# Performance work log

Hardware: AMD Instinct MI355X
Metric: run time of the kernel (lower is better)

## Reference

```python
import jax, jax.numpy as jnp
import numpy as np
import math

DIM = 1024
HEADS = 16
B, N = 2, 2048

POLY = jnp.array([-0.037, 0.481, -2.3, 4.917, -1.791], dtype=jnp.float32)


def adaptive_temperature_softmax(logits):
    # logits: [b, h, n, n]
    original_probs = jax.nn.softmax(logits, axis=-1)
    entropy = jnp.sum(-original_probs * jnp.log(original_probs + 1e-9), axis=-1, keepdims=True)
    e2 = entropy * entropy
    poly_result = POLY[0] * e2 * e2 + POLY[1] * e2 * entropy + POLY[2] * e2 + POLY[3] * entropy + POLY[4]
    beta = jnp.where(entropy > 0.5, jnp.maximum(poly_result, 1.0), 1.0)
    return jax.nn.softmax(logits * beta, axis=-1)


def setup_inputs() -> dict:
    key = jax.random.key(0)
    ks = jax.random.split(key, 5)
    s = 1.0 / math.sqrt(DIM)
    return {
        "x": jax.random.normal(ks[0], (B, N, DIM), dtype=jnp.float32),
        "Wq": jax.random.normal(ks[1], (DIM, DIM), dtype=jnp.float32) * s,
        "Wk": jax.random.normal(ks[2], (DIM, DIM), dtype=jnp.float32) * s,
        "Wv": jax.random.normal(ks[3], (DIM, DIM), dtype=jnp.float32) * s,
        "Wo": jax.random.normal(ks[4], (DIM, DIM), dtype=jnp.float32) * s,
        "bo": jnp.zeros((DIM,), dtype=jnp.float32),
    }


def reference(x, Wq, Wk, Wv, Wo, bo):
    b, n, d = x.shape
    h = HEADS
    hd = d // h
    # torch nn.Linear: y = x @ W.T (+ bias)
    def proj(W):
        t = x @ W.T  # [b, n, d]
        return t.reshape(b, n, h, hd).transpose(0, 2, 1, 3)  # [b, h, n, hd]
    q, k, v = proj(Wq), proj(Wk), proj(Wv)
    sim = jnp.einsum('bhid,bhjd->bhij', q, k) / math.sqrt(hd)
    neg = -jnp.finfo(sim.dtype).max
    causal = jnp.triu(jnp.ones((n, n), dtype=bool), k=1)  # True above diagonal
    sim = jnp.where(causal, neg, sim)
    attn = adaptive_temperature_softmax(sim)
    out = jnp.einsum('bhij,bhjd->bhid', attn, v)
    out = out.transpose(0, 2, 1, 3).reshape(b, n, d)
    return out @ Wo.T + bo
```

## Files before the change

### kernel.cpp

```cpp
#include <hip/hip_runtime.h>
#include <math.h>

#define B_   2
#define N_   2048
#define D_   1024
#define H_   16
#define HD_  64
#define BH_  32
#define M_   4096

typedef __bf16 bf16x8 __attribute__((ext_vector_type(8)));
typedef float  f32x4  __attribute__((ext_vector_type(4)));
typedef __attribute__((address_space(3))) uint  lds_u32;
typedef __attribute__((address_space(1))) uint  glob_u32;

__device__ inline unsigned short f2b(float f) {
    unsigned u = __float_as_uint(f);
    u += 0x7FFFu + ((u >> 16) & 1u);
    return (unsigned short)(u >> 16);
}
__device__ inline unsigned short f2b_fast(float f) {
    return (unsigned short)((__float_as_uint(f) + 0x8000u) >> 16);
}

__global__ __launch_bounds__(256)
void cvt_all(const float* __restrict__ x,  const float* __restrict__ wq,
             const float* __restrict__ wk, const float* __restrict__ wv,
             const float* __restrict__ wo, ushort* __restrict__ dst)
{
    int i = blockIdx.x * 256 + threadIdx.x;
    if (i >= 2097152) return;
    int fi = i * 4;
    const float* s; int off;
    if (fi < 4194304) { s = x; off = fi; }
    else {
        int r = fi - 4194304;
        int wsel = r >> 20;
        off = r & 1048575;
        s = (wsel == 0) ? wq : (wsel == 1) ? wk : (wsel == 2) ? wv : wo;
    }
    float4 f = *(const float4*)(s + off);
    ushort4 o;
    o.x = f2b(f.x); o.y = f2b(f.y); o.z = f2b(f.z); o.w = f2b(f.w);
    *(ushort4*)(dst + fi) = o;
}

template <int MODE>
__global__ __launch_bounds__(256)
void gemm_mfma(const ushort* __restrict__ A,
               const ushort* __restrict__ W0, const ushort* __restrict__ W1,
               const ushort* __restrict__ W2, const float* __restrict__ bias,
               ushort* __restrict__ O0, ushort* __restrict__ O1,
               ushort* __restrict__ O2, float* __restrict__ Of)
{
    const int z = blockIdx.z;
    const ushort* W = (z == 0) ? W0 : (z == 1) ? W1 : W2;

    __shared__ alignas(16) ushort As[128][32];
    __shared__ alignas(16) ushort Bs[128][32];

    const int t = threadIdx.x;
    const int lane = t & 63, w = t >> 6;
    const int quad = lane >> 4, l15 = lane & 15;
    const int wm = (w >> 1) * 64, wn = (w & 1) * 64;
    const int tileM = blockIdx.x * 128, tileN = blockIdx.y * 128;
    const int crow = lane >> 2;
    const int ccol = (lane & 3) * 8;

    f32x4 acc[4][4];
#pragma unroll
    for (int mt = 0; mt < 4; ++mt)
#pragma unroll
        for (int nt = 0; nt < 4; ++nt) acc[mt][nt] = (f32x4){0.f, 0.f, 0.f, 0.f};

    for (int k0 = 0; k0 < D_; k0 += 32) {
        __syncthreads();
#pragma unroll
        for (int cc = 0; cc < 2; ++cc) {
            int ch = w * 2 + cc;
            const ushort* ga = &A[(size_t)(tileM + ch * 16 + crow) * D_ + k0 + ccol];
            __builtin_amdgcn_global_load_lds((const glob_u32*)ga, (lds_u32*)&As[ch * 16][0], 16, 0, 0);
            const ushort* gb = &W[(size_t)(tileN + ch * 16 + crow) * D_ + k0 + ccol];
            __builtin_amdgcn_global_load_lds((const glob_u32*)gb, (lds_u32*)&Bs[ch * 16][0], 16, 0, 0);
        }
        __syncthreads();

        bf16x8 af[4], bf[4];
#pragma unroll
        for (int mt = 0; mt < 4; ++mt) af[mt] = *(const bf16x8*)&As[wm + mt * 16 + l15][quad * 8];
#pragma unroll
        for (int nt = 0; nt < 4; ++nt) bf[nt] = *(const bf16x8*)&Bs[wn + nt * 16 + l15][quad * 8];
#pragma unroll
        for (int mt = 0; mt < 4; ++mt)
#pragma unroll
            for (int nt = 0; nt < 4; ++nt)
                acc[mt][nt] = __builtin_amdgcn_mfma_f32_16x16x32_bf16(af[mt], bf[nt], acc[mt][nt], 0, 0, 0);
    }

    ushort* O = (z == 0) ? O0 : (z == 1) ? O1 : O2;
    const float scl = (MODE == 0 && z == 0) ? 0.125f : 1.0f;
#pragma unroll
    for (int mt = 0; mt < 4; ++mt)
#pragma unroll
        for (int nt = 0; nt < 4; ++nt) {
            if (MODE == 0 && z == 2) {
                int rg0 = tileM + wm + mt * 16 + quad * 4;
                int cg  = tileN + wn + nt * 16 + l15;
                int b = rg0 >> 11, n0 = rg0 & (N_ - 1);
                int h = cg >> 6, dd = cg & 63;
                ushort4 o4;
                o4.x = f2b(acc[mt][nt][0]); o4.y = f2b(acc[mt][nt][1]);
                o4.z = f2b(acc[mt][nt][2]); o4.w = f2b(acc[mt][nt][3]);
                *(ushort4*)&O[((size_t)((b * H_ + h) * HD_ + dd)) * N_ + n0] = o4;
            } else {
#pragma unroll
                for (int r = 0; r < 4; ++r) {
                    int rg = tileM + wm + mt * 16 + quad * 4 + r;
                    int cg = tileN + wn + nt * 16 + l15;
                    float v = acc[mt][nt][r];
                    if (MODE == 0) {
                        int b = rg >> 11, n = rg & (N_ - 1);
                        int h = cg >> 6, dd = cg & 63;
                        O[(((size_t)(b * H_ + h)) * N_ + n) * HD_ + dd] = f2b(v * scl);
                    } else {
                        Of[(size_t)rg * D_ + cg] = v + bias[cg];
                    }
                }
            }
        }
}

__global__ __launch_bounds__(256)
void attn_mfma(const ushort* __restrict__ Q, const ushort* __restrict__ K,
               const ushort* __restrict__ VT, ushort* __restrict__ AO)
{
    const int bid = blockIdx.x;
    const int qt = 31 - (bid >> 5);
    const int bh = bid & 31;
    const size_t kvbase = (size_t)bh * N_ * HD_;

    __shared__ alignas(16) ushort Ks[64][72];
    __shared__ alignas(16) ushort Vt[64][72];
    __shared__ alignas(16) ushort Ps[4][4][296];

    const int t = threadIdx.x;
    const int lane = t & 63, w = t >> 6;
    const int quad = lane >> 4, l15 = lane & 15;
    const float SH = 8.0f;

    const int skey = t >> 3;
    const int skc  = (t & 7) * 8;
    const ushort* KS0 = K  + kvbase + (size_t)skey * HD_ + skc;
    const ushort* KS1 = KS0 + 32 * HD_;
    const ushort* VS0 = VT + kvbase + (size_t)skey * N_ + skc;
    const ushort* VS1 = VS0 + 32 * N_;

    bf16x8 aq0, aq1;
    {
        const size_t qr = kvbase + (size_t)(qt * 64 + w * 16 + l15) * HD_;
        aq0 = *(const bf16x8*)&Q[qr + quad * 8];
        aq1 = *(const bf16x8*)&Q[qr + 32 + quad * 8];
    }
    const int qrow = w * 16 + quad * 4;

    float ez[4] = {0.f, 0.f, 0.f, 0.f};
    float sz[4] = {0.f, 0.f, 0.f, 0.f};

    uint4 pk0 = *(const uint4*)KS0;
    uint4 pk1 = *(const uint4*)KS1;
    for (int kb = 0; kb <= qt; ++kb) {
        __syncthreads();
        *(uint4*)&Ks[skey][skc]      = pk0;
        *(uint4*)&Ks[32 + skey][skc] = pk1;
        __syncthreads();
        if (kb < qt) {
            pk0 = *(const uint4*)(KS0 + (size_t)(kb + 1) * (64 * HD_));
            pk1 = *(const uint4*)(KS1 + (size_t)(kb + 1) * (64 * HD_));
        }
        if (kb < qt) {
#pragma unroll
            for (int nt = 0; nt < 4; ++nt) {
                f32x4 sv = (f32x4){0.f, 0.f, 0.f, 0.f};
                sv = __builtin_amdgcn_mfma_f32_16x16x32_bf16(aq0, *(const bf16x8*)&Ks[nt * 16 + l15][quad * 8], sv, 0, 0, 0);
                sv = __builtin_amdgcn_mfma_f32_16x16x32_bf16(aq1, *(const bf16x8*)&Ks[nt * 16 + l15][32 + quad * 8], sv, 0, 0, 0);
#pragma unroll
                for (int r = 0; r < 4; ++r) {
                    float sh = sv[r] - SH;
                    float e = __expf(sh);
                    ez[r] += e;
                    sz[r] = fmaf(e, sh, sz[r]);
                }
            }
        } else {
#pragma unroll
            for (int nt = 0; nt < 4; ++nt) {
                f32x4 sv = (f32x4){0.f, 0.f, 0.f, 0.f};
                sv = __builtin_amdgcn_mfma_f32_16x16x32_bf16(aq0, *(const bf16x8*)&Ks[nt * 16 + l15][quad * 8], sv, 0, 0, 0);
                sv = __builtin_amdgcn_mfma_f32_16x16x32_bf16(aq1, *(const bf16x8*)&Ks[nt * 16 + l15][32 + quad * 8], sv, 0, 0, 0);
                const int kcol = nt * 16 + l15;
#pragma unroll
                for (int r = 0; r < 4; ++r) {
                    float sh = sv[r] - SH;
                    float e = (kcol <= qrow + r) ? __expf(sh) : 0.f;
                    ez[r] += e;
                    sz[r] = fmaf(e, sh, sz[r]);
                }
            }
        }
    }
#pragma unroll
    for (int r = 0; r < 4; ++r) {
#pragma unroll
        for (int off = 1; off < 16; off <<= 1) {
            ez[r] += __shfl_xor(ez[r], off);
            sz[r] += __shfl_xor(sz[r], off);
        }
    }

    float nbs[4], bl[4];
#pragma unroll
    for (int r = 0; r < 4; ++r) {
        float Z = ez[r];
        float Hh = __logf(Z) - sz[r] / Z;
        float bb = 1.f;
        if (Hh > 0.5f) {
            float e2 = Hh * Hh;
            float p = -0.037f * e2 * e2 + 0.481f * e2 * Hh - 2.3f * e2 + 4.917f * Hh - 1.791f;
            bb = fmaxf(p, 1.f);
        }
        bl[r] = bb;
        nbs[r] = -bb * SH;
    }

    f32x4 ov[4];
#pragma unroll
    for (int nt = 0; nt < 4; ++nt) ov[nt] = (f32x4){0.f, 0.f, 0.f, 0.f};
    float zp[4] = {0.f, 0.f, 0.f, 0.f};

    pk0 = *(const uint4*)KS0;
    pk1 = *(const uint4*)KS1;
    uint4 pv0 = *(const uint4*)VS0;
    uint4 pv1 = *(const uint4*)VS1;
    for (int kb = 0; kb <= qt; ++kb) {
        __syncthreads();
        *(uint4*)&Ks[skey][skc]      = pk0;
        *(uint4*)&Ks[32 + skey][skc] = pk1;
        *(uint4*)&Vt[skey][skc]      = pv0;
        *(uint4*)&Vt[32 + skey][skc] = pv1;
        __syncthreads();
        if (kb < qt) {
            pk0 = *(const uint4*)(KS0 + (size_t)(kb + 1) * (64 * HD_));
            pk1 = *(const uint4*)(KS1 + (size_t)(kb + 1) * (64 * HD_));
            pv0 = *(const uint4*)(VS0 + (kb + 1) * 64);
            pv1 = *(const uint4*)(VS1 + (kb + 1) * 64);
        }
        const bool diag = (kb == qt);

        float wv[4][4];
#pragma unroll
        for (int nt = 0; nt < 4; ++nt) {
            f32x4 sv = (f32x4){0.f, 0.f, 0.f, 0.f};
            sv = __builtin_amdgcn_mfma_f32_16x16x32_bf16(aq0, *(const bf16x8*)&Ks[nt * 16 + l15][quad * 8], sv, 0, 0, 0);
            sv = __builtin_amdgcn_mfma_f32_16x16x32_bf16(aq1, *(const bf16x8*)&Ks[nt * 16 + l15][32 + quad * 8], sv, 0, 0, 0);
            const int kcol = nt * 16 + l15;
#pragma unroll
            for (int r = 0; r < 4; ++r) {
                float e = __expf(fmaf(bl[r], sv[r], nbs[r]));
                wv[nt][r] = (!diag || (kcol <= qrow + r)) ? e : 0.f;
            }
        }
#pragma unroll
        for (int nt = 0; nt < 4; ++nt)
#pragma unroll
            for (int r = 0; r < 4; ++r)
                Ps[w][quad][r * 72 + nt * 16 + l15] = f2b_fast(wv[nt][r]);
#pragma unroll
        for (int r = 0; r < 4; ++r)
            zp[r] += (wv[0][r] + wv[1][r]) + (wv[2][r] + wv[3][r]);

        bf16x8 pa0 = *(const bf16x8*)&Ps[w][l15 >> 2][(l15 & 3) * 72 + quad * 8];
        bf16x8 pa1 = *(const bf16x8*)&Ps[w][l15 >> 2][(l15 & 3) * 72 + 32 + quad * 8];
#pragma unroll
        for (int nt = 0; nt < 4; ++nt) {
            ov[nt] = __builtin_amdgcn_mfma_f32_16x16x32_bf16(pa0, *(const bf16x8*)&Vt[nt * 16 + l15][quad * 8], ov[nt], 0, 0, 0);
            ov[nt] = __builtin_amdgcn_mfma_f32_16x16x32_bf16(pa1, *(const bf16x8*)&Vt[nt * 16 + l15][32 + quad * 8], ov[nt], 0, 0, 0);
        }
    }
#pragma unroll
    for (int r = 0; r < 4; ++r)
#pragma unroll
        for (int off = 1; off < 16; off <<= 1) zp[r] += __shfl_xor(zp[r], off);

    const int b = bh >> 4, h = bh & 15;
#pragma unroll
    for (int r = 0; r < 4; ++r) {
        int qg = qt * 64 + w * 16 + quad * 4 + r;
        float inv = 1.f / zp[r];
        size_t rowoff = ((size_t)(b * N_ + qg)) * D_ + h * HD_;
#pragma unroll
        for (int nt = 0; nt < 4; ++nt)
            AO[rowoff + nt * 16 + l15] = f2b(ov[nt][r] * inv);
    }
}

extern "C" void kernel_launch(void* const* d_in, const int* in_sizes, int n_in,
                              void* d_out, int out_size, void* d_ws, size_t ws_size,
                              hipStream_t stream)
{
    const float* x  = (const float*)d_in[0];
    const float* Wq = (const float*)d_in[1];
    const float* Wk = (const float*)d_in[2];
    const float* Wv = (const float*)d_in[3];
    const float* Wo = (const float*)d_in[4];
    const float* bo = (const float*)d_in[5];
    float* out = (float*)d_out;

    ushort* ws  = (ushort*)d_ws;
    ushort* xb  = ws;
    ushort* wqb = ws + 4194304;
    ushort* wkb = ws + 5242880;
    ushort* wvb = ws + 6291456;
    ushort* wob = ws + 7340032;
    ushort* Qb  = ws + 8388608;
    ushort* Kb  = ws + 12582912;
    ushort* Vtb = ws + 16777216;
    ushort* aob = ws + 20971520;

    cvt_all<<<8192, 256, 0, stream>>>(x, Wq, Wk, Wv, Wo, xb);

    gemm_mfma<0><<<dim3(32, 8, 3), 256, 0, stream>>>(
        xb, wqb, wkb, wvb, nullptr, Qb, Kb, Vtb, nullptr);

    attn_mfma<<<dim3(1024), 256, 0, stream>>>(Qb, Kb, Vtb, aob);

    gemm_mfma<1><<<dim3(32, 8, 1), 256, 0, stream>>>(
        aob, wob, nullptr, nullptr, bo, nullptr, nullptr, nullptr, out);
}
```

Measured before the change: 217.0 us.

## Register-prefetch GEMM tiles with padded LDS and split output GEMM into smaller tiles

```diff
diff --git a/kernel.cpp b/kernel.cpp
--- a/kernel.cpp
+++ b/kernel.cpp
@@ -11,8 +11,6 @@
 
 typedef __bf16 bf16x8 __attribute__((ext_vector_type(8)));
 typedef float  f32x4  __attribute__((ext_vector_type(4)));
-typedef __attribute__((address_space(3))) uint  lds_u32;
-typedef __attribute__((address_space(1))) uint  glob_u32;
 
 __device__ inline unsigned short f2b(float f) {
     unsigned u = __float_as_uint(f);
@@ -45,27 +43,31 @@
     *(ushort4*)(dst + fi) = o;
 }
 
-template <int MODE>
 __global__ __launch_bounds__(256)
-void gemm_mfma(const ushort* __restrict__ A,
-               const ushort* __restrict__ W0, const ushort* __restrict__ W1,
-               const ushort* __restrict__ W2, const float* __restrict__ bias,
-               ushort* __restrict__ O0, ushort* __restrict__ O1,
-               ushort* __restrict__ O2, float* __restrict__ Of)
+void gemm_qkv(const ushort* __restrict__ A,
+              const ushort* __restrict__ W0, const ushort* __restrict__ W1,
+              const ushort* __restrict__ W2,
+              ushort* __restrict__ O0, ushort* __restrict__ O1,
+              ushort* __restrict__ O2)
 {
     const int z = blockIdx.z;
     const ushort* W = (z == 0) ? W0 : (z == 1) ? W1 : W2;
 
-    __shared__ alignas(16) ushort As[128][32];
-    __shared__ alignas(16) ushort Bs[128][32];
+    __shared__ alignas(16) ushort As[128][40];
+    __shared__ alignas(16) ushort Bs[128][40];
 
     const int t = threadIdx.x;
     const int lane = t & 63, w = t >> 6;
     const int quad = lane >> 4, l15 = lane & 15;
     const int wm = (w >> 1) * 64, wn = (w & 1) * 64;
     const int tileM = blockIdx.x * 128, tileN = blockIdx.y * 128;
-    const int crow = lane >> 2;
-    const int ccol = (lane & 3) * 8;
+
+    const int r0 = t >> 2, r1 = 64 + (t >> 2);
+    const int cg = (t & 3) * 8;
+    const ushort* GA0 = A + (size_t)(tileM + r0) * D_ + cg;
+    const ushort* GA1 = A + (size_t)(tileM + r1) * D_ + cg;
+    const ushort* GB0 = W + (size_t)(tileN + r0) * D_ + cg;
+    const ushort* GB1 = W + (size_t)(tileN + r1) * D_ + cg;
 
     f32x4 acc[4][4];
 #pragma unroll
@@ -73,17 +75,22 @@
 #pragma unroll
         for (int nt = 0; nt < 4; ++nt) acc[mt][nt] = (f32x4){0.f, 0.f, 0.f, 0.f};
 
+    uint4 pa0 = *(const uint4*)GA0, pa1 = *(const uint4*)GA1;
+    uint4 pb0 = *(const uint4*)GB0, pb1 = *(const uint4*)GB1;
+
     for (int k0 = 0; k0 < D_; k0 += 32) {
         __syncthreads();
-#pragma unroll
-        for (int cc = 0; cc < 2; ++cc) {
-            int ch = w * 2 + cc;
-            const ushort* ga = &A[(size_t)(tileM + ch * 16 + crow) * D_ + k0 + ccol];
-            __builtin_amdgcn_global_load_lds((const glob_u32*)ga, (lds_u32*)&As[ch * 16][0], 16, 0, 0);
-            const ushort* gb = &W[(size_t)(tileN + ch * 16 + crow) * D_ + k0 + ccol];
-            __builtin_amdgcn_global_load_lds((const glob_u32*)gb, (lds_u32*)&Bs[ch * 16][0], 16, 0, 0);
-        }
-        __syncthreads();
+        *(uint4*)&As[r0][cg] = pa0;
+        *(uint4*)&As[r1][cg] = pa1;
+        *(uint4*)&Bs[r0][cg] = pb0;
+        *(uint4*)&Bs[r1][cg] = pb1;
+        __syncthreads();
+        if (k0 + 32 < D_) {
+            pa0 = *(const uint4*)(GA0 + k0 + 32);
+            pa1 = *(const uint4*)(GA1 + k0 + 32);
+            pb0 = *(const uint4*)(GB0 + k0 + 32);
+            pb1 = *(const uint4*)(GB1 + k0 + 32);
+        }
 
         bf16x8 af[4], bf[4];
 #pragma unroll
@@ -98,16 +105,16 @@
     }
 
     ushort* O = (z == 0) ? O0 : (z == 1) ? O1 : O2;
-    const float scl = (MODE == 0 && z == 0) ? 0.125f : 1.0f;
+    const float scl = (z == 0) ? 0.125f : 1.0f;
 #pragma unroll
     for (int mt = 0; mt < 4; ++mt)
 #pragma unroll
         for (int nt = 0; nt < 4; ++nt) {
-            if (MODE == 0 && z == 2) {
+            if (z == 2) {
                 int rg0 = tileM + wm + mt * 16 + quad * 4;
-                int cg  = tileN + wn + nt * 16 + l15;
+                int cgc = tileN + wn + nt * 16 + l15;
                 int b = rg0 >> 11, n0 = rg0 & (N_ - 1);
-                int h = cg >> 6, dd = cg & 63;
+                int h = cgc >> 6, dd = cgc & 63;
                 ushort4 o4;
                 o4.x = f2b(acc[mt][nt][0]); o4.y = f2b(acc[mt][nt][1]);
                 o4.z = f2b(acc[mt][nt][2]); o4.w = f2b(acc[mt][nt][3]);
@@ -116,18 +123,77 @@
 #pragma unroll
                 for (int r = 0; r < 4; ++r) {
                     int rg = tileM + wm + mt * 16 + quad * 4 + r;
-                    int cg = tileN + wn + nt * 16 + l15;
-                    float v = acc[mt][nt][r];
-                    if (MODE == 0) {
-                        int b = rg >> 11, n = rg & (N_ - 1);
-                        int h = cg >> 6, dd = cg & 63;
-                        O[(((size_t)(b * H_ + h)) * N_ + n) * HD_ + dd] = f2b(v * scl);
-                    } else {
-                        Of[(size_t)rg * D_ + cg] = v + bias[cg];
-                    }
+                    int cgc = tileN + wn + nt * 16 + l15;
+                    int b = rg >> 11, n = rg & (N_ - 1);
+                    int h = cgc >> 6, dd = cgc & 63;
+                    O[(((size_t)(b * H_ + h)) * N_ + n) * HD_ + dd] = f2b(acc[mt][nt][r] * scl);
                 }
             }
         }
+}
+
+__global__ __launch_bounds__(256)
+void gemm_fin(const ushort* __restrict__ A, const ushort* __restrict__ W,
+              const float* __restrict__ bias, float* __restrict__ Of)
+{
+    __shared__ alignas(16) ushort As[128][40];
+    __shared__ alignas(16) ushort Bs[64][40];
+
+    const int t = threadIdx.x;
+    const int lane = t & 63, w = t >> 6;
+    const int quad = lane >> 4, l15 = lane & 15;
+    const int wm = (w >> 1) * 64, wn = (w & 1) * 32;
+    const int tileM = blockIdx.x * 128, tileN = blockIdx.y * 64;
+
+    const int r0 = t >> 2, r1 = 64 + (t >> 2);
+    const int cg = (t & 3) * 8;
+    const ushort* GA0 = A + (size_t)(tileM + r0) * D_ + cg;
+    const ushort* GA1 = A + (size_t)(tileM + r1) * D_ + cg;
+    const ushort* GB0 = W + (size_t)(tileN + r0) * D_ + cg;
+
+    f32x4 acc[4][2];
+#pragma unroll
+    for (int mt = 0; mt < 4; ++mt)
+#pragma unroll
+        for (int nt = 0; nt < 2; ++nt) acc[mt][nt] = (f32x4){0.f, 0.f, 0.f, 0.f};
+
+    uint4 pa0 = *(const uint4*)GA0, pa1 = *(const uint4*)GA1;
+    uint4 pb0 = *(const uint4*)GB0;
+
+    for (int k0 = 0; k0 < D_; k0 += 32) {
+        __syncthreads();
+        *(uint4*)&As[r0][cg] = pa0;
+        *(uint4*)&As[r1][cg] = pa1;
+        *(uint4*)&Bs[r0 & 63][cg] = pb0;
+        __syncthreads();
+        if (k0 + 32 < D_) {
+            pa0 = *(const uint4*)(GA0 + k0 + 32);
+            pa1 = *(const uint4*)(GA1 + k0 + 32);
+            pb0 = *(const uint4*)(GB0 + k0 + 32);
+        }
+
+        bf16x8 af[4], bf[2];
+#pragma unroll
+        for (int mt = 0; mt < 4; ++mt) af[mt] = *(const bf16x8*)&As[wm + mt * 16 + l15][quad * 8];
+#pragma unroll
+        for (int nt = 0; nt < 2; ++nt) bf[nt] = *(const bf16x8*)&Bs[wn + nt * 16 + l15][quad * 8];
+#pragma unroll
+        for (int mt = 0; mt < 4; ++mt)
+#pragma unroll
+            for (int nt = 0; nt < 2; ++nt)
+                acc[mt][nt] = __builtin_amdgcn_mfma_f32_16x16x32_bf16(af[mt], bf[nt], acc[mt][nt], 0, 0, 0);
+    }
+
+#pragma unroll
+    for (int mt = 0; mt < 4; ++mt)
+#pragma unroll
+        for (int nt = 0; nt < 2; ++nt)
+#pragma unroll
+            for (int r = 0; r < 4; ++r) {
+                int rg = tileM + wm + mt * 16 + quad * 4 + r;
+                int cgc = tileN + wn + nt * 16 + l15;
+                Of[(size_t)rg * D_ + cgc] = acc[mt][nt][r] + bias[cgc];
+            }
 }
 
 __global__ __launch_bounds__(256)
@@ -328,11 +394,10 @@
 
     cvt_all<<<8192, 256, 0, stream>>>(x, Wq, Wk, Wv, Wo, xb);
 
-    gemm_mfma<0><<<dim3(32, 8, 3), 256, 0, stream>>>(
-        xb, wqb, wkb, wvb, nullptr, Qb, Kb, Vtb, nullptr);
+    gemm_qkv<<<dim3(32, 8, 3), 256, 0, stream>>>(
+        xb, wqb, wkb, wvb, Qb, Kb, Vtb);
 
     attn_mfma<<<dim3(1024), 256, 0, stream>>>(Qb, Kb, Vtb, aob);
 
-    gemm_mfma<1><<<dim3(32, 8, 1), 256, 0, stream>>>(
-        aob, wob, nullptr, nullptr, bo, nullptr, nullptr, nullptr, out);
-}
+    gemm_fin<<<dim3(32, 16), 256, 0, stream>>>(aob, wob, bo, out);
+}
```

New measurement: 205.8 us. 1.05x faster.
